# Optimization experiments

Hardware: AMD Instinct MI355X
Metric: run time of the kernel (lower is better)

Reference implementation:

```python
import jax, jax.numpy as jnp
import numpy as np

EPSILON = 0.001
PROXIMITY_THRESHOLD = 0.15


def setup_inputs() -> dict:
    key = jax.random.key(0)
    k1, k2, k3 = jax.random.split(key, 3)
    B, N, E = 8, 512, 4096
    node_positions = jax.random.uniform(k1, (B, N, 2), dtype=jnp.float32)
    adjacency = jax.random.normal(k2, (B, N, N), dtype=jnp.float32)
    edge_index = jax.random.randint(k3, (2, E), 0, B * N, dtype=jnp.int64)
    return {"node_positions": node_positions, "adjacency": adjacency, "edge_index": edge_index}


def _candidate_mask(pos, src, dst, batch, prox):
    # pos: (BN,2); src/dst/batch: (E,)
    p_src = pos[src]
    p_dst = pos[dst]
    mid = (p_src + p_dst) * 0.5                      # (E,2)
    half = jnp.linalg.norm(p_dst - p_src, axis=-1) * 0.5  # (E,)
    dist = jnp.linalg.norm(mid[:, None] - mid[None, :], axis=-1)  # (E,E)
    reach = half[:, None] + half[None, :] + prox
    E = src.shape[0]
    idx = jnp.arange(E)
    upper = idx[None, :] > idx[:, None]              # ei < ej
    same_batch = batch[:, None] == batch[None, :]
    shares = ((src[:, None] == src[None, :]) | (src[:, None] == dst[None, :])
              | (dst[:, None] == src[None, :]) | (dst[:, None] == dst[None, :]))
    return (dist < reach) & upper & same_batch & ~shares


def _segment_distance_dense(p_src, p_dst):
    # All-pairs closest-approach distance between segments i and j.
    d1 = p_dst - p_src                               # (E,2)
    sq = jnp.maximum((d1 * d1).sum(-1), 1e-12)       # (E,)
    a = sq[:, None]                                  # a_i
    e = sq[None, :]                                  # e_j
    b = d1 @ d1.T                                    # (E,E) d1_i . d1_j
    d1_dot_a1 = (d1 * p_src).sum(-1)                 # (E,) d1_k . a1_k
    c = d1_dot_a1[:, None] - d1 @ p_src.T            # d1_i . (a1_i - b1_j)
    f = p_src @ d1.T - d1_dot_a1[None, :]            # d1_j . (a1_i - b1_j)
    denom = jnp.maximum(a * e - b * b, 1e-12)
    s = (b * f - c * e) / denom
    t = (a * f - b * c) / denom
    s = jnp.clip(s, 0.0, 1.0)
    t = jnp.clip(t, 0.0, 1.0)
    t = jnp.clip((b * s + f) / e, 0.0, 1.0)
    s = jnp.clip((b * t - c) / a, 0.0, 1.0)
    closest_a = p_src[:, None, :] + s[..., None] * d1[:, None, :]   # (E,E,2)
    closest_b = p_src[None, :, :] + t[..., None] * d1[None, :, :]   # (E,E,2)
    return jnp.linalg.norm(closest_a - closest_b, axis=-1)          # (E,E)


def reference(node_positions, adjacency, edge_index):
    # adjacency is accepted (per the torch forward signature) but unused by this axiom.
    B, N, _ = node_positions.shape
    pos = node_positions.reshape(-1, 2)              # (B*N, 2)
    src = edge_index[0]
    dst = edge_index[1]
    batch = src // N                                 # (E,) batch membership per edge
    mask = jax.lax.stop_gradient(
        _candidate_mask(jax.lax.stop_gradient(pos), src, dst, batch, PROXIMITY_THRESHOLD))
    dmin = _segment_distance_dense(pos[src], pos[dst])  # (E,E)
    pair_loss = jax.nn.relu(EPSILON - dmin) * mask.astype(dmin.dtype)
    n_pairs = mask.sum()
    loss = pair_loss.sum() / jnp.maximum(n_pairs, 1).astype(dmin.dtype)
    violation_mask = mask & (pair_loss > 0)
    violation_scores = jax.lax.stop_gradient(pair_loss)
    return loss, violation_mask, violation_scores
```

## Files before the change

kernel.cpp:

```cpp
#include <hip/hip_runtime.h>


#define EDGES   4096
#define LOGE    12
#define EPS     0.001f
#define PROX    0.15f
#define NBUCKET 2048

__global__ __launch_bounds__(256) void edge_pre(
    const float2* __restrict__ pos,
    const int*    __restrict__ esrc,
    const int*    __restrict__ edst,
    float4* __restrict__ rec1, float4* __restrict__ rec2, float4* __restrict__ rec3)
{
#pragma clang fp contract(off)
    const int e = blockIdx.x * 256 + threadIdx.x;
    const int s = esrc[e], d = edst[e];
    const float2 a1 = pos[s], a2 = pos[d];
    const float d1x = a2.x - a1.x, d1y = a2.y - a1.y;
    const float midx = (a1.x + a2.x) * 0.5f, midy = (a1.y + a2.y) * 0.5f;
    const float half = sqrtf(d1x * d1x + d1y * d1y) * 0.5f;
    const float sq   = fmaxf(d1x * d1x + d1y * d1y, 1e-12f);
    const float dda  = d1x * a1.x + d1y * a1.y;
    rec1[e] = make_float4(a1.x, a1.y, d1x, d1y);
    rec2[e] = make_float4(midx, midy, half, dda);
    rec3[e] = make_float4(sq, __int_as_float(s), __int_as_float(d), 0.0f);
}

__device__ __forceinline__ void pair_math(
    const float4 r1i, const float4 r2i, const float4 r3i,
    const float4 r1j, const float4 r2j, const float4 r3j,
    const bool upper, float& pl, bool& mask)
{
#pragma clang fp contract(off)
    const float dmx  = r2i.x - r2j.x, dmy = r2i.y - r2j.y;
    const float dist = sqrtf(dmx * dmx + dmy * dmy);
    const float reach = r2i.z + r2j.z + PROX;

    const int si = __float_as_int(r3i.y), di_ = __float_as_int(r3i.z);
    const int sj = __float_as_int(r3j.y), dj  = __float_as_int(r3j.z);
    const bool sameb  = (si >> 9) == (sj >> 9);
    const bool shares = (si == sj) | (si == dj) | (di_ == sj) | (di_ == dj);
    mask = (dist < reach) & upper & sameb & (!shares);

    const float sqi = r3i.x, sqj = r3j.x;
    const float b = r1i.z * r1j.z + r1i.w * r1j.w;
    const float c = r2i.w - (r1i.z * r1j.x + r1i.w * r1j.y);
    const float f = (r1i.x * r1j.z + r1i.y * r1j.w) - r2j.w;
    const float denom = fmaxf(sqi * sqj - b * b, 1e-12f);

    float s = (b * f - c * sqj) / denom;
    s = fminf(fmaxf(s, 0.0f), 1.0f);
    const float t = fminf(fmaxf((b * s + f) / sqj, 0.0f), 1.0f);
    s = fminf(fmaxf((b * t - c) / sqi, 0.0f), 1.0f);

    const float cax = r1i.x + s * r1i.z, cay = r1i.y + s * r1i.w;
    const float cbx = r1j.x + t * r1j.z, cby = r1j.y + t * r1j.w;
    const float dx = cax - cbx, dy = cay - cby;
    const float dmin = sqrtf(dx * dx + dy * dy);

    pl = fmaxf(EPS - dmin, 0.0f) * (mask ? 1.0f : 0.0f);
}

__global__ __launch_bounds__(256) void pair_kernel(
    const float4* __restrict__ rec1, const float4* __restrict__ rec2,
    const float4* __restrict__ rec3,
    float*        __restrict__ out,
    float*        __restrict__ bsum,
    unsigned int* __restrict__ bcnt)
{
#pragma clang fp contract(off)
    const int i     = blockIdx.y;
    const int jbase = blockIdx.x << 10;
    const int j0    = jbase + (threadIdx.x << 2);
    const int k0    = (i << LOGE) | j0;

    float* __restrict__ o_mask  = out + 1;
    float* __restrict__ o_score = out + 1 + EDGES * EDGES;

    if (jbase + 1023 <= i) {
        #pragma unroll
        for (int u = 0; u < 4; ++u) { o_mask[k0 + u] = 0.0f; o_score[k0 + u] = 0.0f; }
        return;
    }

    const float4 r1i = rec1[i], r2i = rec2[i], r3i = rec3[i];

    float vsum = 0.0f;
    int   vcnt = 0;
    #pragma unroll
    for (int u = 0; u < 4; ++u) {
        const int j = j0 + u;
        float pl; bool mask;
        pair_math(r1i, r2i, r3i, rec1[j], rec2[j], rec3[j], j > i, pl, mask);
        o_mask[k0 + u]  = (mask && pl > 0.0f) ? 1.0f : 0.0f;
        o_score[k0 + u] = pl;
        vsum += pl;
        vcnt += mask ? 1 : 0;
    }

    #pragma unroll
    for (int off = 32; off > 0; off >>= 1) {
        vsum += __shfl_xor(vsum, off, 64);
        vcnt += __shfl_xor(vcnt, off, 64);
    }
    __shared__ float    ls[4];
    __shared__ unsigned lc[4];
    const int wid = threadIdx.x >> 6, lane = threadIdx.x & 63;
    if (lane == 0) { ls[wid] = vsum; lc[wid] = (unsigned)vcnt; }
    __syncthreads();
    if (threadIdx.x == 0) {
        const float    s4 = ls[0] + ls[1] + ls[2] + ls[3];
        const unsigned c4 = lc[0] + lc[1] + lc[2] + lc[3];
        if (s4 != 0.0f || c4 != 0u) {
            const int bk = ((blockIdx.y << 2) | blockIdx.x) & (NBUCKET - 1);
            atomicAdd(&bsum[bk], s4);
            atomicAdd(&bcnt[bk], c4);
        }
    }
}

__global__ __launch_bounds__(256) void finalize_kernel(
    const float* __restrict__ bsum, const unsigned* __restrict__ bcnt,
    float* __restrict__ out)
{
    float    s = 0.0f;
    unsigned c = 0u;
    for (int b = threadIdx.x; b < NBUCKET; b += 256) { s += bsum[b]; c += bcnt[b]; }
    #pragma unroll
    for (int off = 32; off > 0; off >>= 1) {
        s += __shfl_xor(s, off, 64);
        c += (unsigned)__shfl_xor((int)c, off, 64);
    }
    __shared__ float    ls[4];
    __shared__ unsigned lc[4];
    const int wid = threadIdx.x >> 6, lane = threadIdx.x & 63;
    if (lane == 0) { ls[wid] = s; lc[wid] = c; }
    __syncthreads();
    if (threadIdx.x == 0) {
        const float    st = ls[0] + ls[1] + ls[2] + ls[3];
        const unsigned ct = lc[0] + lc[1] + lc[2] + lc[3];
        const unsigned n  = ct > 1u ? ct : 1u;
        out[0] = st / (float)n;
    }
}

extern "C" void kernel_launch(void* const* d_in, const int* in_sizes, int n_in,
                              void* d_out, int out_size, void* d_ws, size_t ws_size,
                              hipStream_t stream) {
    const float2* pos  = (const float2*)d_in[0];
    const int*    esrc = (const int*)d_in[2];
    const int*    edst = esrc + EDGES;

    float*        out  = (float*)d_out;
    float*        bsum = (float*)d_ws;
    unsigned int* bcnt = (unsigned int*)((float*)d_ws + NBUCKET);
    float4*       rec1 = (float4*)((char*)d_ws + NBUCKET * 8);
    float4*       rec2 = rec1 + EDGES;
    float4*       rec3 = rec2 + EDGES;

    hipMemsetAsync(d_ws, 0, NBUCKET * 2 * sizeof(float), stream);

    edge_pre<<<EDGES / 256, 256, 0, stream>>>(pos, esrc, edst, rec1, rec2, rec3);
    dim3 grid(4, EDGES);
    pair_kernel<<<grid, 256, 0, stream>>>(rec1, rec2, rec3, out, bsum, bcnt);
    finalize_kernel<<<1, 256, 0, stream>>>(bsum, bcnt, out);
}
```

Measured before the change: 188.3 us.

## Tile pair kernel over 8 rows per block and reuse j records

Each block now handles 8 i-rows by 512 j-columns instead of 1 row by 1024 columns. Each thread keeps its two j-records in registers and reuses them across the 8 rows. Stores change from 4 consecutive floats per thread to one float per thread per row, still coalesced across the wave. This cuts redundant j-record loads and the block count, at the cost of coarser skipping of the lower triangle and more registers per thread. The kernel is likely bound by the 128MB of output writes, so the gain may be small.

```diff
diff --git a/kernel.cpp b/kernel.cpp
--- a/kernel.cpp
+++ b/kernel.cpp
@@ -6,6 +6,8 @@
 #define EPS     0.001f
 #define PROX    0.15f
 #define NBUCKET 2048
+#define ITILE   8
+#define JBLK    512
 
 __global__ __launch_bounds__(256) void edge_pre(
     const float2* __restrict__ pos,
@@ -70,33 +72,50 @@
     unsigned int* __restrict__ bcnt)
 {
 #pragma clang fp contract(off)
-    const int i     = blockIdx.y;
-    const int jbase = blockIdx.x << 10;
-    const int j0    = jbase + (threadIdx.x << 2);
-    const int k0    = (i << LOGE) | j0;
+    const int ibase = blockIdx.y * ITILE;
+    const int jbase = blockIdx.x * JBLK;
+    const int tid   = threadIdx.x;
 
     float* __restrict__ o_mask  = out + 1;
     float* __restrict__ o_score = out + 1 + EDGES * EDGES;
 
-    if (jbase + 1023 <= i) {
+    if (jbase + JBLK - 1 <= ibase) {
         #pragma unroll
-        for (int u = 0; u < 4; ++u) { o_mask[k0 + u] = 0.0f; o_score[k0 + u] = 0.0f; }
+        for (int ii = 0; ii < ITILE; ++ii) {
+            const int row = (ibase + ii) << LOGE;
+            o_mask [row + jbase + tid]       = 0.0f;
+            o_score[row + jbase + tid]       = 0.0f;
+            o_mask [row + jbase + 256 + tid] = 0.0f;
+            o_score[row + jbase + 256 + tid] = 0.0f;
+        }
         return;
     }
 
-    const float4 r1i = rec1[i], r2i = rec2[i], r3i = rec3[i];
+    const int j0 = jbase + tid;
+    const int j1 = j0 + 256;
+    const float4 r1j0 = rec1[j0], r2j0 = rec2[j0], r3j0 = rec3[j0];
+    const float4 r1j1 = rec1[j1], r2j1 = rec2[j1], r3j1 = rec3[j1];
 
     float vsum = 0.0f;
     int   vcnt = 0;
-    #pragma unroll
-    for (int u = 0; u < 4; ++u) {
-        const int j = j0 + u;
-        float pl; bool mask;
-        pair_math(r1i, r2i, r3i, rec1[j], rec2[j], rec3[j], j > i, pl, mask);
-        o_mask[k0 + u]  = (mask && pl > 0.0f) ? 1.0f : 0.0f;
-        o_score[k0 + u] = pl;
-        vsum += pl;
-        vcnt += mask ? 1 : 0;
+
+    #pragma unroll 2
+    for (int ii = 0; ii < ITILE; ++ii) {
+        const int i = ibase + ii;
+        const float4 r1i = rec1[i], r2i = rec2[i], r3i = rec3[i];
+
+        float pl0, pl1; bool m0, m1;
+        pair_math(r1i, r2i, r3i, r1j0, r2j0, r3j0, j0 > i, pl0, m0);
+        pair_math(r1i, r2i, r3i, r1j1, r2j1, r3j1, j1 > i, pl1, m1);
+
+        const int row = i << LOGE;
+        o_mask [row + j0] = (m0 && pl0 > 0.0f) ? 1.0f : 0.0f;
+        o_score[row + j0] = pl0;
+        o_mask [row + j1] = (m1 && pl1 > 0.0f) ? 1.0f : 0.0f;
+        o_score[row + j1] = pl1;
+
+        vsum += pl0 + pl1;
+        vcnt += (m0 ? 1 : 0) + (m1 ? 1 : 0);
     }
 
     #pragma unroll
@@ -106,14 +125,14 @@
     }
     __shared__ float    ls[4];
     __shared__ unsigned lc[4];
-    const int wid = threadIdx.x >> 6, lane = threadIdx.x & 63;
+    const int wid = tid >> 6, lane = tid & 63;
     if (lane == 0) { ls[wid] = vsum; lc[wid] = (unsigned)vcnt; }
     __syncthreads();
-    if (threadIdx.x == 0) {
+    if (tid == 0) {
         const float    s4 = ls[0] + ls[1] + ls[2] + ls[3];
         const unsigned c4 = lc[0] + lc[1] + lc[2] + lc[3];
         if (s4 != 0.0f || c4 != 0u) {
-            const int bk = ((blockIdx.y << 2) | blockIdx.x) & (NBUCKET - 1);
+            const int bk = (blockIdx.y * 8 + blockIdx.x) & (NBUCKET - 1);
             atomicAdd(&bsum[bk], s4);
             atomicAdd(&bcnt[bk], c4);
         }
@@ -162,7 +181,7 @@
     hipMemsetAsync(d_ws, 0, NBUCKET * 2 * sizeof(float), stream);
 
     edge_pre<<<EDGES / 256, 256, 0, stream>>>(pos, esrc, edst, rec1, rec2, rec3);
-    dim3 grid(4, EDGES);
+    dim3 grid(EDGES / JBLK, EDGES / ITILE);
     pair_kernel<<<grid, 256, 0, stream>>>(rec1, rec2, rec3, out, bsum, bcnt);
     finalize_kernel<<<1, 256, 0, stream>>>(bsum, bcnt, out);
 }
```

Result: faster. 181.8 us (-3.5%).
